# Kernel optimization log

Hardware: AMD Instinct MI355X
Metric: run time of the kernel (lower is better)

Reference implementation:

```python
import jax, jax.numpy as jnp
import numpy as np

B, N, IN_DIM, HID, OUT, E = 2, 50000, 64, 256, 128, 500000

def setup_inputs() -> dict:
    key = jax.random.key(0)
    ks = jax.random.split(key, 8)
    s = lambda fan_in: 1.0 / np.sqrt(fan_in)
    x = jax.random.normal(ks[0], (B, N, IN_DIM), dtype=jnp.float32)
    edges = jax.random.randint(ks[1], (E, 2), 0, N, dtype=jnp.int64)
    return {
        "x": x,
        "edges": edges,
        "ew1": jax.random.normal(ks[2], (2 * IN_DIM, HID), dtype=jnp.float32) * s(2 * IN_DIM),
        "eb1": jnp.zeros((HID,), jnp.float32),
        "ew2": jax.random.normal(ks[3], (HID, OUT), dtype=jnp.float32) * s(HID),
        "eb2": jnp.zeros((OUT,), jnp.float32),
        "nw1": jax.random.normal(ks[4], (IN_DIM, HID), dtype=jnp.float32) * s(IN_DIM),
        "nb1": jnp.zeros((HID,), jnp.float32),
        "nw2": jax.random.normal(ks[5], (HID, OUT), dtype=jnp.float32) * s(HID),
        "nb2": jnp.zeros((OUT,), jnp.float32),
        "dw": jax.random.normal(ks[6], (OUT, IN_DIM), dtype=jnp.float32) * s(OUT),
        "db": jnp.zeros((IN_DIM,), jnp.float32),
    }

def _mlp(z, w1, b1, w2, b2):
    return jax.nn.relu(z @ w1 + b1) @ w2 + b2

def reference(x, edges, ew1, eb1, ew2, eb2, nw1, nb1, nw2, nb2, dw, db):
    u, v = edges[:, 0], edges[:, 1]
    # node embedding: [B, N, OUT]
    h = _mlp(x, nw1, nb1, nw2, nb2)
    # per-edge MLP on concatenated endpoint features: [B, E, OUT]
    edge_input = jnp.concatenate([x[:, u], x[:, v]], axis=-1)  # [B, E, 2*IN]
    edge_emb = _mlp(edge_input, ew1, eb1, ew2, eb2)
    # scatter-add edge message to both endpoints
    messages = jnp.zeros_like(h).at[:, u].add(edge_emb).at[:, v].add(edge_emb)
    h = h + messages
    recon = h @ dw + db  # [B, N, IN]
    return recon
```

## Files before the change

### kernel.cpp

```cpp
#include <hip/hip_runtime.h>
#include <hip/hip_bf16.h>

#define BB   2
#define NN   50000
#define BN   100000
#define NE   500000
#define NSB  196
#define NODE_NB 1563

using u16 = unsigned short;
using u32 = unsigned int;
typedef __attribute__((ext_vector_type(8))) short short8;
typedef __attribute__((ext_vector_type(8))) _Float16 half8;
typedef __attribute__((ext_vector_type(4))) float f32x4;

__device__ __forceinline__ u16 f2bf(float f) {
    union { float f; u32 u; } w; w.f = f;
    return (u16)((w.u + 0x7fffu + ((w.u >> 16) & 1u)) >> 16);
}
__device__ __forceinline__ u16 f2h(float f) {
    _Float16 h = (_Float16)f; u16 u; __builtin_memcpy(&u, &h, 2); return u;
}

#if defined(__has_builtin)
#if __has_builtin(__builtin_amdgcn_cvt_pk_bf16_f32)
#define HAVE_CVTPK 1
#endif
#if __has_builtin(__builtin_amdgcn_cvt_pkrtz)
#define HAVE_PKRTZ 1
#endif
#endif

__device__ __forceinline__ u32 pack_bf(float lo, float hi) {
#ifdef HAVE_CVTPK
    auto r = __builtin_amdgcn_cvt_pk_bf16_f32(lo, hi);
    u32 out; __builtin_memcpy(&out, &r, sizeof(out));
    return out;
#else
    return ((u32)f2bf(hi) << 16) | (u32)f2bf(lo);
#endif
}

__device__ __forceinline__ u32 pack_h2(float lo, float hi) {
#ifdef HAVE_PKRTZ
    auto r = __builtin_amdgcn_cvt_pkrtz(lo, hi);
    u32 out; __builtin_memcpy(&out, &r, sizeof(out));
    return out;
#else
    return ((u32)f2h(hi) << 16) | (u32)f2h(lo);
#endif
}

__device__ __forceinline__ u32 pk_add_h2(u32 a, u32 b) {
    u32 d; asm("v_pk_add_f16 %0, %1, %2" : "=v"(d) : "v"(a), "v"(b)); return d;
}
__device__ __forceinline__ u32 pk_relu_h2(u32 a) {
    u32 d, z = 0u;
    asm("v_pk_max_f16 %0, %1, %2" : "=v"(d) : "v"(a), "v"(z)); return d;
}
__device__ __forceinline__ half8 as_h8(short8 s) {
    half8 h; __builtin_memcpy(&h, &s, 16); return h;
}

__global__ __launch_bounds__(256) void weight_prep_hist(
    const float* __restrict__ ew1, const float* __restrict__ nw1,
    const float* __restrict__ ew2, const float* __restrict__ nw2,
    const float* __restrict__ dw,  const float* __restrict__ db,
    const float* __restrict__ eb2, const float* __restrict__ nb2,
    const int* __restrict__ edges, int* __restrict__ curU, int* __restrict__ curV,
    u16* __restrict__ frag, float* __restrict__ bias2)
{
    int blk = blockIdx.x, t = threadIdx.x;
    if (blk >= 321) {
        int e = (blk - 321) * 256 + t;
        if (e < NE) {
            atomicAdd(&curU[edges[2*e]], 1);
            atomicAdd(&curV[edges[2*e+1]], 1);
        }
        return;
    }
    if (blk < 192) {
        int idx = blk * 256 + t;
        const float* src; int KB, local;
        if (idx < 32768) { local = idx;         src = ew1; KB = 4; }
        else             { local = idx - 32768; src = nw1; KB = 2; }
        int j = local & 7, l = (local >> 3) & 63, rest = local >> 9;
        int kblk = rest % KB, ntile = rest / KB;
        int n = ntile * 16 + (l & 15);
        int k = kblk * 32 + ((l >> 4) << 3) + j;
        frag[idx] = f2bf(src[k * 256 + n]);
    } else if (blk < 320) {
        int idx = (blk - 192) * 256 + t;
        bool is_e = (idx < 16384);
        const float* src = is_e ? ew2 : nw2;
        int local = idx & 16383;
        int j = local & 7, l = (local >> 3) & 63, rest = local >> 9;
        int kblk = rest & 7, ntile = rest >> 3;
        int n = ntile * 16 + (l & 15);
        int k = kblk * 32 + ((l >> 4) << 3) + j;
        float s = 0.f;
        for (int jj = 0; jj < 128; ++jj) s = fmaf(src[k * 128 + jj], dw[jj * 64 + n], s);
        frag[49152 + idx] = is_e ? f2h(s) : f2bf(s);
    } else if (t < 128) {
        int d = t & 63;
        const float* bsrc = (t >= 64) ? nb2 : eb2;
        float s = 0.f;
        #pragma unroll 4
        for (int j = 0; j < 128; ++j) s = fmaf(bsrc[j], dw[j * 64 + d], s);
        if (t >= 64) bias2[64 + d] = s + db[d];
        else         bias2[d] = s;
    }
}

__global__ __launch_bounds__(256) void scan_pass2d(const int* __restrict__ bsum2,
                                                   int* __restrict__ boff2) {
    __shared__ int s[256];
    const int t = threadIdx.x;
    const int base = blockIdx.y * (NSB + 1);
    s[t] = (t < NSB) ? bsum2[base + t] : 0;
    __syncthreads();
    for (int d = 1; d < 256; d <<= 1) {
        int v = (t >= d) ? s[t - d] : 0;
        __syncthreads();
        s[t] += v;
        __syncthreads();
    }
    if (t <= NSB) boff2[base + t] = (t == 0) ? 0 : s[t - 1];
}

__global__ __launch_bounds__(256) void scan_pass3d(int* __restrict__ curU,
                                                   int* __restrict__ curV,
                                                   const int* __restrict__ boff2,
                                                   int* __restrict__ uoff,
                                                   int* __restrict__ voff) {
    __shared__ int s[256];
    const int t = threadIdx.x;
    int* cursor = blockIdx.y ? curV : curU;
    int* off    = blockIdx.y ? voff : uoff;
    const int base = blockIdx.y * (NSB + 1);
    int i = blockIdx.x * 256 + t;
    int v = (i < NN) ? cursor[i] : 0;
    s[t] = v;
    __syncthreads();
    for (int d = 1; d < 256; d <<= 1) {
        int p = (t >= d) ? s[t - d] : 0;
        __syncthreads();
        s[t] += p;
        __syncthreads();
    }
    int excl = boff2[base + blockIdx.x] + s[t] - v;
    if (i < NN) { off[i] = excl; cursor[i] = excl; }
    if (i == NN - 1) off[NN] = excl + v;
}

__global__ __launch_bounds__(256) void csr_fill2(const int* __restrict__ edges,
                                                 int* __restrict__ curU,
                                                 int* __restrict__ curV,
                                                 int2* __restrict__ uv,
                                                 int* __restrict__ vmap) {
    int e = blockIdx.x * 256 + threadIdx.x;
    if (e < NE) {
        int u = edges[2*e], v = edges[2*e+1];
        int s0 = atomicAdd(&curU[u], 1);
        uv[s0] = make_int2(u, v);
        int s1 = atomicAdd(&curV[v], 1);
        vmap[s1] = s0;
    }
}

__global__ __launch_bounds__(256) void node_mlp_kernel(
    const float* __restrict__ x, const float* __restrict__ nb1,
    const float* __restrict__ eb1, const float* __restrict__ bias2,
    const u16* __restrict__ frag,
    u16* __restrict__ At, u16* __restrict__ Ab, float* __restrict__ out,
    const int* __restrict__ curU, const int* __restrict__ curV,
    int* __restrict__ bsum2)
{
    __shared__ u16 xs[64 * 64];
    __shared__ u16 hid[64 * 128];
    const int t = threadIdx.x;

    if (blockIdx.x >= NODE_NB) {
        int sb = blockIdx.x - NODE_NB;
        int y = sb / NSB, xi = sb - y * NSB;
        const int* cursor = y ? curV : curU;
        int* s = (int*)xs;
        int i = xi * 256 + t;
        s[t] = (i < NN) ? cursor[i] : 0;
        __syncthreads();
        for (int d = 128; d > 0; d >>= 1) {
            if (t < d) s[t] += s[t + d];
            __syncthreads();
        }
        if (t == 0) bsum2[y * (NSB + 1) + xi] = s[0];
        return;
    }

    const int wave = t >> 6, l = t & 63, lane15 = l & 15, quad = l >> 4;
    const int r0 = blockIdx.x * 64;
    const int valid = min(64, BN - r0);

    #pragma unroll
    for (int it = 0; it < 4; ++it) {
        int i = t + it * 256;
        int m = i >> 4, c4 = i & 15;
        int row = min(r0 + m, BN - 1);
        float4 g = ((const float4*)x)[(size_t)row * 16 + c4];
        uint2 q = make_uint2(pack_bf(g.x, g.y), pack_bf(g.z, g.w));
        int chunk = c4 >> 1;
        *(uint2*)(xs + m * 64 + ((chunk ^ (m & 7)) << 3) + (c4 & 1) * 4) = q;
    }
    __syncthreads();

    f32x4 acc2[4];
    #pragma unroll
    for (int mt = 0; mt < 4; ++mt) acc2[mt] = f32x4{0.f,0.f,0.f,0.f};
    const u16* w1n = frag + 32768;
    const u16* w2n = frag + 65536;
    #pragma unroll
    for (int H = 0; H < 2; ++H) {
        f32x4 acc1[2][4];
        #pragma unroll
        for (int i = 0; i < 2; ++i)
            #pragma unroll
            for (int mt = 0; mt < 4; ++mt) acc1[i][mt] = f32x4{0.f,0.f,0.f,0.f};
        #pragma unroll
        for (int kblk = 0; kblk < 2; ++kblk) {
            short8 bf[4], af[2];
            int chunk = kblk * 4 + quad;
            #pragma unroll
            for (int mt = 0; mt < 4; ++mt) {
                int row = mt*16 + lane15;
                bf[mt] = *(const short8*)(xs + row * 64 + ((chunk ^ (row & 7)) << 3));
            }
            #pragma unroll
            for (int i = 0; i < 2; ++i)
                af[i] = *(const short8*)(w1n + (((H*8 + wave*2 + i)*2 + kblk)*64 + l) * 8);
            #pragma unroll
            for (int i = 0; i < 2; ++i)
                #pragma unroll
                for (int mt = 0; mt < 4; ++mt)
                    acc1[i][mt] = __builtin_amdgcn_mfma_f32_16x16x32_bf16(af[i], bf[mt], acc1[i][mt], 0, 0, 0);
        }
        #pragma unroll
        for (int i = 0; i < 2; ++i) {
            int ntl = wave*2 + i;
            int n0 = (H*8 + ntl)*16 + quad*4;
            int c16 = ntl*2 + (quad >> 1);
            float4 bv = *(const float4*)(nb1 + n0);
            #pragma unroll
            for (int mt = 0; mt < 4; ++mt) {
                int row = mt*16 + lane15;
                uint2 q = make_uint2(
                    pack_bf(fmaxf(acc1[i][mt][0] + bv.x, 0.f), fmaxf(acc1[i][mt][1] + bv.y, 0.f)),
                    pack_bf(fmaxf(acc1[i][mt][2] + bv.z, 0.f), fmaxf(acc1[i][mt][3] + bv.w, 0.f)));
                *(uint2*)(hid + row * 128 + ((c16 ^ (row & 15)) << 3) + (quad & 1) * 4) = q;
            }
        }
        __syncthreads();
        #pragma unroll
        for (int kb = 0; kb < 4; ++kb) {
            short8 bf[4], af;
            int chunk = kb * 4 + quad;
            #pragma unroll
            for (int mt = 0; mt < 4; ++mt) {
                int row = mt*16 + lane15;
                bf[mt] = *(const short8*)(hid + row * 128 + ((chunk ^ (row & 15)) << 3));
            }
            af = *(const short8*)(w2n + ((wave*8 + H*4 + kb)*64 + l) * 8);
            #pragma unroll
            for (int mt = 0; mt < 4; ++mt)
                acc2[mt] = __builtin_amdgcn_mfma_f32_16x16x32_bf16(af, bf[mt], acc2[mt], 0, 0, 0);
        }
        __syncthreads();
    }
    {
        int n0 = wave*16 + quad*4;
        float4 bv = *(const float4*)(bias2 + 64 + n0);
        #pragma unroll
        for (int mt = 0; mt < 4; ++mt) {
            int m = mt*16 + lane15;
            if (m < valid) {
                float4 o;
                o.x = acc2[mt][0] + bv.x; o.y = acc2[mt][1] + bv.y;
                o.z = acc2[mt][2] + bv.z; o.w = acc2[mt][3] + bv.w;
                *(float4*)(out + (size_t)(r0 + m) * 64 + n0) = o;
            }
        }
    }

    const u16* w1e = frag;
    #pragma unroll
    for (int T = 0; T < 2; ++T) {
        u16* dst = T ? Ab : At;
        #pragma unroll
        for (int H = 0; H < 2; ++H) {
            f32x4 acc[2][4];
            #pragma unroll
            for (int i = 0; i < 2; ++i)
                #pragma unroll
                for (int mt = 0; mt < 4; ++mt) acc[i][mt] = f32x4{0.f,0.f,0.f,0.f};
            #pragma unroll
            for (int kblk = 0; kblk < 2; ++kblk) {
                short8 bf[4], af[2];
                int chunk = kblk * 4 + quad;
                #pragma unroll
                for (int mt = 0; mt < 4; ++mt) {
                    int row = mt*16 + lane15;
                    bf[mt] = *(const short8*)(xs + row * 64 + ((chunk ^ (row & 7)) << 3));
                }
                #pragma unroll
                for (int i = 0; i < 2; ++i)
                    af[i] = *(const short8*)(w1e + (((H*8 + wave*2 + i)*4 + T*2 + kblk)*64 + l) * 8);
                #pragma unroll
                for (int i = 0; i < 2; ++i)
                    #pragma unroll
                    for (int mt = 0; mt < 4; ++mt)
                        acc[i][mt] = __builtin_amdgcn_mfma_f32_16x16x32_bf16(af[i], bf[mt], acc[i][mt], 0, 0, 0);
            }
            #pragma unroll
            for (int i = 0; i < 2; ++i) {
                int ntl = wave*2 + i;
                int n0 = (H*8 + ntl)*16 + quad*4;
                int c16 = ntl*2 + (quad >> 1);
                float4 bv;
                if (T == 0) bv = *(const float4*)(eb1 + n0);
                else        bv = make_float4(0.f, 0.f, 0.f, 0.f);
                #pragma unroll
                for (int mt = 0; mt < 4; ++mt) {
                    int row = mt*16 + lane15;
                    uint2 q = make_uint2(
                        pack_h2(acc[i][mt][0] + bv.x, acc[i][mt][1] + bv.y),
                        pack_h2(acc[i][mt][2] + bv.z, acc[i][mt][3] + bv.w));
                    *(uint2*)(hid + row * 128 + ((c16 ^ (row & 15)) << 3) + (quad & 1) * 4) = q;
                }
            }
            __syncthreads();
            #pragma unroll
            for (int it = 0; it < 4; ++it) {
                int i = t + it * 256;
                int m = i >> 4, c = i & 15;
                if (m < valid)
                    ((uint4*)dst)[((size_t)(r0 + m)) * 32 + H*16 + c] =
                        *(const uint4*)(hid + m * 128 + ((c ^ (m & 15)) << 3));
            }
            __syncthreads();
        }
    }
}

__global__ __launch_bounds__(256) void edge_emb3_kernel(
    const u16* __restrict__ At, const u16* __restrict__ Ab,
    const int2* __restrict__ uv, const float* __restrict__ bias2,
    const u16* __restrict__ frag, u16* __restrict__ perm)
{
    __shared__ u16 hid[64 * 128];
    __shared__ int us[64], vs[64];
    const int t = threadIdx.x;
    const int wave = t >> 6, l = t & 63, lane15 = l & 15, quad = l >> 4;
    const int e0 = blockIdx.x * 64;
    const int valid = min(64, NE - e0);

    if (t < 64) {
        int2 p = uv[min(e0 + t, NE - 1)];
        us[t] = p.x;
        vs[t] = p.y;
    }
    __syncthreads();

    const u16* w2 = frag + 49152;
    f32x4 accB[2][4];
    #pragma unroll
    for (int b = 0; b < 2; ++b)
        #pragma unroll
        for (int mt = 0; mt < 4; ++mt) accB[b][mt] = f32x4{0.f,0.f,0.f,0.f};

    #pragma unroll
    for (int b = 0; b < 2; ++b) {
        const u16* Atb = At + (size_t)b * NN * 256;
        const u16* Abb = Ab + (size_t)b * NN * 256;
        #pragma unroll
        for (int half = 0; half < 2; ++half) {
            #pragma unroll
            for (int it = 0; it < 4; ++it) {
                int i = t + it * 256;
                int m = i >> 4, c = i & 15;
                int cg = half * 16 + c;
                int u = us[m], v = vs[m];
                uint4 a = ((const uint4*)Atb)[(size_t)((u32)u) * 32 + cg];
                uint4 bq = ((const uint4*)Abb)[(size_t)((u32)v) * 32 + cg];
                uint4 r;
                r.x = pk_relu_h2(pk_add_h2(a.x, bq.x));
                r.y = pk_relu_h2(pk_add_h2(a.y, bq.y));
                r.z = pk_relu_h2(pk_add_h2(a.z, bq.z));
                r.w = pk_relu_h2(pk_add_h2(a.w, bq.w));
                *(uint4*)(hid + m * 128 + ((c ^ (m & 15)) << 3)) = r;
            }
            __syncthreads();
            #pragma unroll
            for (int kb = 0; kb < 4; ++kb) {
                short8 bf[4], af;
                int chunk = kb * 4 + quad;
                #pragma unroll
                for (int mt = 0; mt < 4; ++mt) {
                    int row = mt*16 + lane15;
                    bf[mt] = *(const short8*)(hid + row * 128 + ((chunk ^ (row & 15)) << 3));
                }
                af = *(const short8*)(w2 + ((wave*8 + half*4 + kb)*64 + l) * 8);
                #pragma unroll
                for (int mt = 0; mt < 4; ++mt)
                    accB[b][mt] = __builtin_amdgcn_mfma_f32_16x16x32_f16(as_h8(af), as_h8(bf[mt]), accB[b][mt], 0, 0, 0);
            }
            __syncthreads();
        }
    }

    {
        int n0 = wave*16 + quad*4;
        float4 bv = *(const float4*)(bias2 + n0);
        #pragma unroll
        for (int b = 0; b < 2; ++b) {
            int cc = b*8 + wave*2 + (quad >> 1);
            #pragma unroll
            for (int mt = 0; mt < 4; ++mt) {
                int m = mt*16 + lane15;
                uint2 q = make_uint2(
                    pack_bf(accB[b][mt][0] + bv.x, accB[b][mt][1] + bv.y),
                    pack_bf(accB[b][mt][2] + bv.z, accB[b][mt][3] + bv.w));
                *(uint2*)(hid + m * 128 + ((cc ^ (m & 15)) << 3) + (quad & 1) * 4) = q;
            }
        }
    }
    __syncthreads();

    #pragma unroll
    for (int it = 0; it < 4; ++it) {
        int i = t + it * 256;
        int m = i >> 4, c = i & 15;
        if (m < valid)
            ((uint4*)perm)[((size_t)(e0 + m)) * 16 + c] =
                *(const uint4*)(hid + m * 128 + ((c ^ (m & 15)) << 3));
    }
}

#define ACCUM8(q) { union { u32 u; float f; } xx;                         \
    xx.u = (q).x << 16;          a0 += xx.f;                              \
    xx.u = (q).x & 0xffff0000u;  a1 += xx.f;                              \
    xx.u = (q).y << 16;          a2 += xx.f;                              \
    xx.u = (q).y & 0xffff0000u;  a3 += xx.f;                              \
    xx.u = (q).z << 16;          a4 += xx.f;                              \
    xx.u = (q).z & 0xffff0000u;  a5 += xx.f;                              \
    xx.u = (q).w << 16;          a6 += xx.f;                              \
    xx.u = (q).w & 0xffff0000u;  a7 += xx.f; }

__global__ __launch_bounds__(256) void gather4_kernel(
    const u32* __restrict__ perm32, const int* __restrict__ uoff,
    const int* __restrict__ voff, const int* __restrict__ vmap,
    float* __restrict__ out)
{
    const int t = threadIdx.x, wave = t >> 6, l = t & 63;
    const int n = blockIdx.x * 4 + wave;
    const int ub = uoff[n], ucnt = uoff[n + 1] - ub;
    const int vb = voff[n], vcnt = voff[n + 1] - vb;
    if ((ucnt | vcnt) == 0) return;
    const int sg = l >> 4, c16 = l & 15;
    float a0=0.f,a1=0.f,a2=0.f,a3=0.f,a4=0.f,a5=0.f,a6=0.f,a7=0.f;

    for (int j0 = 0; j0 < ucnt; j0 += 8) {
        int jA = j0 + sg, jB = j0 + 4 + sg;
        uint4 qA = *(const uint4*)(perm32 + (size_t)(ub + min(jA, ucnt - 1)) * 64 + c16 * 4);
        uint4 qB = *(const uint4*)(perm32 + (size_t)(ub + min(jB, ucnt - 1)) * 64 + c16 * 4);
        if (jA < ucnt) ACCUM8(qA);
        if (jB < ucnt) ACCUM8(qB);
    }
    for (int j0 = 0; j0 < vcnt; j0 += 8) {
        int jA = j0 + sg, jB = j0 + 4 + sg;
        int pA = vmap[vb + min(jA, vcnt - 1)];
        int pB = vmap[vb + min(jB, vcnt - 1)];
        uint4 qA = *(const uint4*)(perm32 + (size_t)pA * 64 + c16 * 4);
        uint4 qB = *(const uint4*)(perm32 + (size_t)pB * 64 + c16 * 4);
        if (jA < vcnt) ACCUM8(qA);
        if (jB < vcnt) ACCUM8(qB);
    }

    a0 += __shfl_xor(a0, 16); a1 += __shfl_xor(a1, 16);
    a2 += __shfl_xor(a2, 16); a3 += __shfl_xor(a3, 16);
    a4 += __shfl_xor(a4, 16); a5 += __shfl_xor(a5, 16);
    a6 += __shfl_xor(a6, 16); a7 += __shfl_xor(a7, 16);
    a0 += __shfl_xor(a0, 32); a1 += __shfl_xor(a1, 32);
    a2 += __shfl_xor(a2, 32); a3 += __shfl_xor(a3, 32);
    a4 += __shfl_xor(a4, 32); a5 += __shfl_xor(a5, 32);
    a6 += __shfl_xor(a6, 32); a7 += __shfl_xor(a7, 32);

    if (l < 16) {
        float* p = out + ((size_t)((l >> 3) * NN + n)) * 64 + (l & 7) * 8;
        float4 h0 = *(float4*)p, h1 = *(float4*)(p + 4);
        h0.x += a0; h0.y += a1; h0.z += a2; h0.w += a3;
        h1.x += a4; h1.y += a5; h1.z += a6; h1.w += a7;
        *(float4*)p = h0; *(float4*)(p + 4) = h1;
    }
}

extern "C" void kernel_launch(void* const* d_in, const int* in_sizes, int n_in,
                              void* d_out, int out_size, void* d_ws, size_t ws_size,
                              hipStream_t stream) {
    const float* x     = (const float*)d_in[0];
    const int*   edges = (const int*)d_in[1];
    const float* ew1   = (const float*)d_in[2];
    const float* eb1   = (const float*)d_in[3];
    const float* ew2   = (const float*)d_in[4];
    const float* eb2   = (const float*)d_in[5];
    const float* nw1   = (const float*)d_in[6];
    const float* nb1   = (const float*)d_in[7];
    const float* nw2   = (const float*)d_in[8];
    const float* nb2   = (const float*)d_in[9];
    const float* dw    = (const float*)d_in[10];
    const float* db    = (const float*)d_in[11];
    float* out = (float*)d_out;

    char* w = (char*)d_ws;
    size_t o = 0;
    auto take = [&](size_t bytes) { char* p = w + o; o = (o + bytes + 511) & ~(size_t)511; return p; };
    u16*   frag   = (u16*)  take(81920 * 2);
    float* bias2  = (float*)take(128 * 4);
    int*   curU   = (int*)  take((size_t)NN * 4);
    int*   curV   = (int*)  take((size_t)NN * 4);
    int*   uoff   = (int*)  take((size_t)(NN + 1) * 4);
    int*   voff   = (int*)  take((size_t)(NN + 1) * 4);
    int*   bsum2  = (int*)  take((size_t)2 * (NSB + 1) * 4);
    int*   boff2  = (int*)  take((size_t)2 * (NSB + 1) * 4);
    int*   vmap   = (int*)  take((size_t)NE * 4);
    int2*  uv     = (int2*) take((size_t)NE * 8);
    u16*   At     = (u16*)  take((size_t)BN * 256 * 2);
    u16*   Ab     = (u16*)  take((size_t)BN * 256 * 2);
    u16*   perm   = (u16*)  take((size_t)NE * 128 * 2);
    (void)ws_size;

    hipMemsetAsync(curU, 0, (size_t)NN * 4, stream);
    hipMemsetAsync(curV, 0, (size_t)NN * 4, stream);

    weight_prep_hist<<<321 + (NE + 255) / 256, 256, 0, stream>>>(
        ew1, nw1, ew2, nw2, dw, db, eb2, nb2, edges, curU, curV, frag, bias2);

    node_mlp_kernel<<<NODE_NB + 2 * NSB, 256, 0, stream>>>(
        x, nb1, eb1, bias2, frag, At, Ab, out, curU, curV, bsum2);

    scan_pass2d<<<dim3(1, 2), 256, 0, stream>>>(bsum2, boff2);
    scan_pass3d<<<dim3(NSB, 2), 256, 0, stream>>>(curU, curV, boff2, uoff, voff);
    csr_fill2<<<(NE + 255) / 256, 256, 0, stream>>>(edges, curU, curV, uv, vmap);

    edge_emb3_kernel<<<(NE + 63) / 64, 256, 0, stream>>>(At, Ab, uv, bias2, frag, perm);

    gather4_kernel<<<NN / 4, 256, 0, stream>>>((const u32*)perm, uoff, voff, vmap, out);
}
```

Measured before the change: 407.3 us.

## Make edge MLP wave-private with register prefetch of next gather phase

Each wave now owns 16 edges and a private LDS slice, so the block-wide __syncthreads barriers are gone. The wave loops over all four output tiles, where before each wave took one tile across 64 edges. The gathered At/Ab rows for the next phase are loaded into registers while the current phase is combined and multiplied, overlapping gather latency with MFMA work. The cost is more VGPRs for the double-buffered prefetch and for loading the weight fragments four times per k-step.

Result: slower. 446.4 us (+9.6%).

```diff
diff --git a/kernel.cpp b/kernel.cpp
--- a/kernel.cpp
+++ b/kernel.cpp
@@ -349,97 +349,103 @@
     }
 }
 
-__global__ __launch_bounds__(256) void edge_emb3_kernel(
+__global__ __launch_bounds__(256) void edge_emb4_kernel(
     const u16* __restrict__ At, const u16* __restrict__ Ab,
     const int2* __restrict__ uv, const float* __restrict__ bias2,
     const u16* __restrict__ frag, u16* __restrict__ perm)
 {
     __shared__ u16 hid[64 * 128];
-    __shared__ int us[64], vs[64];
     const int t = threadIdx.x;
     const int wave = t >> 6, l = t & 63, lane15 = l & 15, quad = l >> 4;
-    const int e0 = blockIdx.x * 64;
-    const int valid = min(64, NE - e0);
-
-    if (t < 64) {
-        int2 p = uv[min(e0 + t, NE - 1)];
-        us[t] = p.x;
-        vs[t] = p.y;
-    }
-    __syncthreads();
+    const int e0w = blockIdx.x * 64 + wave * 16;
+    const int evalid = min(16, NE - e0w);
+
+    int2 puv = uv[min(e0w + lane15, NE - 1)];
+    const u32 ubase = (u32)puv.x * 32;
+    const u32 vbase = (u32)puv.y * 32;
+    u16* hw = hid + wave * 16 * 128;
+
+    const uint4* atp0 = (const uint4*)At;
+    const uint4* atp1 = (const uint4*)(At + (size_t)NN * 256);
+    const uint4* abp0 = (const uint4*)Ab;
+    const uint4* abp1 = (const uint4*)(Ab + (size_t)NN * 256);
 
     const u16* w2 = frag + 49152;
-    f32x4 accB[2][4];
+    f32x4 acc[2][4];
     #pragma unroll
     for (int b = 0; b < 2; ++b)
         #pragma unroll
-        for (int mt = 0; mt < 4; ++mt) accB[b][mt] = f32x4{0.f,0.f,0.f,0.f};
-
-    #pragma unroll
-    for (int b = 0; b < 2; ++b) {
-        const u16* Atb = At + (size_t)b * NN * 256;
-        const u16* Abb = Ab + (size_t)b * NN * 256;
-        #pragma unroll
-        for (int half = 0; half < 2; ++half) {
-            #pragma unroll
-            for (int it = 0; it < 4; ++it) {
-                int i = t + it * 256;
-                int m = i >> 4, c = i & 15;
-                int cg = half * 16 + c;
-                int u = us[m], v = vs[m];
-                uint4 a = ((const uint4*)Atb)[(size_t)((u32)u) * 32 + cg];
-                uint4 bq = ((const uint4*)Abb)[(size_t)((u32)v) * 32 + cg];
-                uint4 r;
-                r.x = pk_relu_h2(pk_add_h2(a.x, bq.x));
-                r.y = pk_relu_h2(pk_add_h2(a.y, bq.y));
-                r.z = pk_relu_h2(pk_add_h2(a.z, bq.z));
-                r.w = pk_relu_h2(pk_add_h2(a.w, bq.w));
-                *(uint4*)(hid + m * 128 + ((c ^ (m & 15)) << 3)) = r;
-            }
-            __syncthreads();
-            #pragma unroll
-            for (int kb = 0; kb < 4; ++kb) {
-                short8 bf[4], af;
-                int chunk = kb * 4 + quad;
-                #pragma unroll
-                for (int mt = 0; mt < 4; ++mt) {
-                    int row = mt*16 + lane15;
-                    bf[mt] = *(const short8*)(hid + row * 128 + ((chunk ^ (row & 15)) << 3));
-                }
-                af = *(const short8*)(w2 + ((wave*8 + half*4 + kb)*64 + l) * 8);
-                #pragma unroll
-                for (int mt = 0; mt < 4; ++mt)
-                    accB[b][mt] = __builtin_amdgcn_mfma_f32_16x16x32_f16(as_h8(af), as_h8(bf[mt]), accB[b][mt], 0, 0, 0);
-            }
-            __syncthreads();
-        }
-    }
+        for (int ntl = 0; ntl < 4; ++ntl) acc[b][ntl] = f32x4{0.f,0.f,0.f,0.f};
+
+    uint4 paA[4], pbA[4], paB[4], pbB[4];
+
+    #pragma unroll
+    for (int it = 0; it < 4; ++it) {
+        paA[it] = atp0[ubase + quad + 4*it];
+        pbA[it] = abp0[vbase + quad + 4*it];
+    }
+
+#define EDGE_PHASE(BB_, HH_, CA, CB, DO_PRE, NA, NB, PAT, PAB, PH_)          \
+    {                                                                         \
+        if (DO_PRE) {                                                         \
+            _Pragma("unroll")                                                 \
+            for (int it = 0; it < 4; ++it) {                                  \
+                NA[it] = PAT[ubase + (PH_)*16 + quad + 4*it];                 \
+                NB[it] = PAB[vbase + (PH_)*16 + quad + 4*it];                 \
+            }                                                                 \
+        }                                                                     \
+        _Pragma("unroll")                                                     \
+        for (int it = 0; it < 4; ++it) {                                      \
+            uint4 r;                                                          \
+            r.x = pk_relu_h2(pk_add_h2(CA[it].x, CB[it].x));                  \
+            r.y = pk_relu_h2(pk_add_h2(CA[it].y, CB[it].y));                  \
+            r.z = pk_relu_h2(pk_add_h2(CA[it].z, CB[it].z));                  \
+            r.w = pk_relu_h2(pk_add_h2(CA[it].w, CB[it].w));                  \
+            int c = quad + 4*it;                                              \
+            *(uint4*)(hw + lane15 * 128 + ((c ^ lane15) << 3)) = r;           \
+        }                                                                     \
+        _Pragma("unroll")                                                     \
+        for (int kb = 0; kb < 4; ++kb) {                                      \
+            short8 bf = *(const short8*)(hw + lane15 * 128 +                  \
+                                         (((kb*4 + quad) ^ lane15) << 3));    \
+            _Pragma("unroll")                                                 \
+            for (int ntl = 0; ntl < 4; ++ntl) {                               \
+                short8 af = *(const short8*)(w2 + ((ntl*8 + (HH_)*4 + kb)*64 + l) * 8); \
+                acc[BB_][ntl] = __builtin_amdgcn_mfma_f32_16x16x32_f16(       \
+                    as_h8(af), as_h8(bf), acc[BB_][ntl], 0, 0, 0);            \
+            }                                                                 \
+        }                                                                     \
+    }
+
+    EDGE_PHASE(0, 0, paA, pbA, 1, paB, pbB, atp0, abp0, 1)
+    EDGE_PHASE(0, 1, paB, pbB, 1, paA, pbA, atp1, abp1, 0)
+    EDGE_PHASE(1, 0, paA, pbA, 1, paB, pbB, atp1, abp1, 1)
+    EDGE_PHASE(1, 1, paB, pbB, 0, paA, pbA, atp0, abp0, 0)
+#undef EDGE_PHASE
 
     {
-        int n0 = wave*16 + quad*4;
-        float4 bv = *(const float4*)(bias2 + n0);
-        #pragma unroll
-        for (int b = 0; b < 2; ++b) {
-            int cc = b*8 + wave*2 + (quad >> 1);
-            #pragma unroll
-            for (int mt = 0; mt < 4; ++mt) {
-                int m = mt*16 + lane15;
+        int n0 = quad * 4;
+        #pragma unroll
+        for (int ntl = 0; ntl < 4; ++ntl) {
+            float4 bv = *(const float4*)(bias2 + ntl*16 + n0);
+            #pragma unroll
+            for (int b = 0; b < 2; ++b) {
+                int cc = b*8 + ntl*2 + (quad >> 1);
                 uint2 q = make_uint2(
-                    pack_bf(accB[b][mt][0] + bv.x, accB[b][mt][1] + bv.y),
-                    pack_bf(accB[b][mt][2] + bv.z, accB[b][mt][3] + bv.w));
-                *(uint2*)(hid + m * 128 + ((cc ^ (m & 15)) << 3) + (quad & 1) * 4) = q;
-            }
-        }
-    }
-    __syncthreads();
+                    pack_bf(acc[b][ntl][0] + bv.x, acc[b][ntl][1] + bv.y),
+                    pack_bf(acc[b][ntl][2] + bv.z, acc[b][ntl][3] + bv.w));
+                *(uint2*)(hw + lane15 * 128 + ((cc ^ lane15) << 3) + (quad & 1) * 4) = q;
+            }
+        }
+    }
 
     #pragma unroll
     for (int it = 0; it < 4; ++it) {
-        int i = t + it * 256;
-        int m = i >> 4, c = i & 15;
-        if (m < valid)
-            ((uint4*)perm)[((size_t)(e0 + m)) * 16 + c] =
-                *(const uint4*)(hid + m * 128 + ((c ^ (m & 15)) << 3));
+        int row = it * 4 + quad;
+        int c = lane15;
+        if (row < evalid)
+            ((uint4*)perm)[((size_t)(e0w + row)) * 16 + c] =
+                *(const uint4*)(hw + row * 128 + ((c ^ row) << 3));
     }
 }
 
@@ -549,7 +555,7 @@
     scan_pass3d<<<dim3(NSB, 2), 256, 0, stream>>>(curU, curV, boff2, uoff, voff);
     csr_fill2<<<(NE + 255) / 256, 256, 0, stream>>>(edges, curU, curV, uv, vmap);
 
-    edge_emb3_kernel<<<(NE + 63) / 64, 256, 0, stream>>>(At, Ab, uv, bias2, frag, perm);
+    edge_emb4_kernel<<<(NE + 63) / 64, 256, 0, stream>>>(At, Ab, uv, bias2, frag, perm);
 
     gather4_kernel<<<NN / 4, 256, 0, stream>>>((const u32*)perm, uoff, voff, vmap, out);
 }
```
